# Kernel optimization log

Hardware: AMD Instinct MI355X
Metric: run time of the kernel (lower is better)

The kernel has to match this reference:

```python
import jax, jax.numpy as jnp
import numpy as np

E = 768   # embed_dim
N = 12    # num_heads
H = 128   # height
W = 128   # width
D = E // N  # head_dim = 64


def setup_inputs() -> dict:
    key = jax.random.key(0)
    ks = jax.random.split(key, 9)
    s = 0.02
    x = jax.random.normal(ks[0], (1, H * W, E), jnp.float32)
    Wq = jax.random.normal(ks[1], (E, E), jnp.float32) * s
    bq = jnp.zeros((E,), jnp.float32)
    Wk = jax.random.normal(ks[2], (E, E), jnp.float32) * s
    bk = jnp.zeros((E,), jnp.float32)
    Wv = jax.random.normal(ks[3], (E, E), jnp.float32) * s
    bv = jnp.zeros((E,), jnp.float32)
    Wo = jax.random.normal(ks[4], (E, E), jnp.float32) * s
    bo = jnp.zeros((E,), jnp.float32)
    return {"x": x, "Wq": Wq, "bq": bq, "Wk": Wk, "bk": bk,
            "Wv": Wv, "bv": bv, "Wo": Wo, "bo": bo}


def reference(x, Wq, bq, Wk, bk, Wv, bv, Wo, bo):
    # projections (torch Linear: x @ W.T + b)
    q = x @ Wq.T + bq
    k = x @ Wk.T + bk
    v = x @ Wv.T + bv

    # q, k -> (1, N, H, W, D)
    q = q.reshape(1, H, W, N, D).transpose(0, 3, 1, 2, 4)
    k = k.reshape(1, H, W, N, D).transpose(0, 3, 1, 2, 4)

    # --- width-axis attention (per row h) ---
    qr_w = q.transpose(0, 2, 1, 3, 4)  # (1, H, N, W, D)
    kr_w = k.transpose(0, 2, 1, 3, 4)  # (1, H, N, W, D)
    v = v.reshape(1, H, W, N, D).transpose(0, 1, 3, 2, 4)  # (1, H, N, W, D)
    # NOTE: original applies no 1/sqrt(D) scaling
    qk_w = jnp.einsum('bhnwd,bhnvd->bhnwv', qr_w, kr_w)  # (1, H, N, W, W)
    qk_w = jax.nn.softmax(qk_w, axis=-1)
    v = jnp.einsum('bhnwv,bhnvd->bhnwd', qk_w, v)  # (1, H, N, W, D)

    # --- height-axis attention (per column w) ---
    qr_h = q.transpose(0, 3, 1, 2, 4)  # (1, W, N, H, D)
    kr_h = k.transpose(0, 3, 1, 2, 4)  # (1, W, N, H, D)
    v = v.transpose(0, 3, 2, 1, 4)     # (1, W, N, H, D)
    qk_h = jnp.einsum('bwnhd,bwngd->bwnhg', qr_h, kr_h)  # (1, W, N, H, H)
    qk_h = jax.nn.softmax(qk_h, axis=-1)
    out = jnp.einsum('bwnhg,bwngd->bwnhd', qk_h, v)  # (1, W, N, H, D)

    # (1, W, N, H, D) -> (1, H, W, N, D) -> (1, H, W, E)
    out = out.transpose(0, 3, 1, 2, 4).reshape(1, H, W, E)
    out = out @ Wo.T + bo
    return out.reshape(1, H * W, E)
```

## Files before the change

### kernel.cpp

```cpp
#include <hip/hip_runtime.h>

typedef __attribute__((ext_vector_type(4))) float f32x4;
typedef __attribute__((ext_vector_type(8))) unsigned short u16x8;
typedef __attribute__((ext_vector_type(8))) __bf16 bf16x8;

typedef __attribute__((address_space(3))) unsigned lds_u32;
typedef const __attribute__((address_space(1))) unsigned glb_u32;

__device__ __forceinline__ unsigned short f2bf(float f) {
    union { float f; unsigned u; } v; v.f = f;
    unsigned r = v.u + 0x7fffu + ((v.u >> 16) & 1u);
    return (unsigned short)(r >> 16);
}

__device__ __forceinline__ f32x4 mfma16(u16x8 a, u16x8 b, f32x4 c) {
    return __builtin_amdgcn_mfma_f32_16x16x32_bf16(
        __builtin_bit_cast(bf16x8, a), __builtin_bit_cast(bf16x8, b), c, 0, 0, 0);
}

__device__ __forceinline__ void gload16(const unsigned short* g, unsigned short* l) {
    __builtin_amdgcn_global_load_lds((glb_u32*)g, (lds_u32*)l, 16, 0, 0);
}

#define BARM() asm volatile("s_barrier" ::: "memory")
#define WAITVM0() asm volatile("s_waitcnt vmcnt(0)" ::: "memory")

__global__ void cvt_f32_bf16(const float* __restrict__ src,
                             unsigned short* __restrict__ dst, int n) {
    int stride = gridDim.x * blockDim.x * 4;
    for (int i = (blockIdx.x * blockDim.x + threadIdx.x) * 4; i < n; i += stride) {
        float4 f = *reinterpret_cast<const float4*>(src + i);
        ushort4 o;
        o.x = f2bf(f.x); o.y = f2bf(f.y); o.z = f2bf(f.z); o.w = f2bf(f.w);
        *reinterpret_cast<ushort4*>(dst + i) = o;
    }
}

__global__ void cvt4_f32_bf16(const float* __restrict__ s0, const float* __restrict__ s1,
                              const float* __restrict__ s2, const float* __restrict__ s3,
                              unsigned short* __restrict__ dst, int per) {
    int total = per * 4;
    int stride = gridDim.x * blockDim.x * 4;
    for (int i = (blockIdx.x * blockDim.x + threadIdx.x) * 4; i < total; i += stride) {
        int w = i / per, off = i - w * per;
        const float* s = w == 0 ? s0 : w == 1 ? s1 : w == 2 ? s2 : s3;
        float4 f = *reinterpret_cast<const float4*>(s + off);
        ushort4 o;
        o.x = f2bf(f.x); o.y = f2bf(f.y); o.z = f2bf(f.z); o.w = f2bf(f.w);
        *reinterpret_cast<ushort4*>(dst + i) = o;
    }
}

template<bool OUTF32>
__device__ __forceinline__ void gemm_core(
    const unsigned short* __restrict__ A,
    const unsigned short* __restrict__ B,
    const float* __restrict__ b0, const float* __restrict__ b1, const float* __restrict__ b2,
    void* __restrict__ C0, void* __restrict__ C1, void* __restrict__ C2,
    int K, int NBY)
{
    __shared__ char lds[32768];
    const int t = threadIdx.x, lane = t & 63, wave = t >> 6;
    const int wm = wave >> 1, wn = wave & 1;

    const int nwg = gridDim.x;
    const int bid = blockIdx.x;
    const int swzb = (bid & 7) * (nwg >> 3) + (bid >> 3);
    const long m0 = (long)(swzb / NBY) * 128;
    const long n0 = (long)(swzb % NBY) * 128;

    const int NT = K >> 6;

    const int rloc = t >> 3;
    const int cel  = ((t & 7) ^ ((t >> 3) & 7)) << 3;
    const unsigned short* Ab = A + (m0 + rloc) * (long)K + cel;
    const unsigned short* Bb = B + (n0 + rloc) * (long)K + cel;

    auto STAGE = [&](int kt) {
        char* da = lds + (wave << 10);
        char* db = lds + 16384 + (wave << 10);
        const unsigned short* sa = Ab + kt * 64;
        const unsigned short* sb = Bb + kt * 64;
        #pragma unroll
        for (int j = 0; j < 4; ++j) {
            gload16(sa + (long)(j * 32) * K, (unsigned short*)(da + j * 4096));
            gload16(sb + (long)(j * 32) * K, (unsigned short*)(db + j * 4096));
        }
    };

    f32x4 acc[4][4] = {};
    u16x8 af[4][2], bfr[4][2];

    auto LD = [&]() {
        const char* bufA = lds;
        const char* bufB = lds + 16384;
        #pragma unroll
        for (int f = 0; f < 4; ++f)
            #pragma unroll
            for (int kk = 0; kk < 2; ++kk) {
                int ra = wm * 64 + f * 16 + (lane & 15);
                int rb = wn * 64 + f * 16 + (lane & 15);
                int cb = kk * 64 + (lane >> 4) * 16;
                af[f][kk]  = *(const u16x8*)(bufA + ra * 128 + (cb ^ ((ra & 7) << 4)));
                bfr[f][kk] = *(const u16x8*)(bufB + rb * 128 + (cb ^ ((rb & 7) << 4)));
            }
    };

    for (int kt = 0; kt < NT; ++kt) {
        STAGE(kt);
        WAITVM0();
        BARM();
        LD();
        #pragma unroll
        for (int kk = 0; kk < 2; ++kk)
            #pragma unroll
            for (int mi = 0; mi < 4; ++mi)
                #pragma unroll
                for (int nf = 0; nf < 4; ++nf)
                    acc[mi][nf] = mfma16(af[mi][kk], bfr[nf][kk], acc[mi][nf]);
        BARM();
    }

    #pragma unroll
    for (int mi = 0; mi < 4; ++mi)
        #pragma unroll
        for (int nf = 0; nf < 4; ++nf) {
            int coln = (int)n0 + wn * 64 + nf * 16 + (lane & 15);
            int which = coln / 768;
            int nl = coln - which * 768;
            const float* bs = which == 0 ? b0 : (which == 1 ? b1 : b2);
            void* Cp       = which == 0 ? C0 : (which == 1 ? C1 : C2);
            float bias = bs[nl];
            #pragma unroll
            for (int q = 0; q < 4; ++q) {
                long row = m0 + wm * 64 + mi * 16 + ((lane >> 4) << 2) + q;
                float val = acc[mi][nf][q] + bias;
                if (OUTF32) ((float*)Cp)[row * 768 + nl] = val;
                else ((unsigned short*)Cp)[row * 768 + nl] = f2bf(val);
            }
        }
}

__global__ __launch_bounds__(256, 4) void qkv_gemm(
    const unsigned short* __restrict__ A, const unsigned short* __restrict__ B,
    const float* b0, const float* b1, const float* b2,
    void* C0, void* C1, void* C2, int K, int NBY)
{
    gemm_core<false>(A, B, b0, b1, b2, C0, C1, C2, K, NBY);
}

__global__ __launch_bounds__(256, 4) void oproj_gemm(
    const unsigned short* __restrict__ A, const unsigned short* __restrict__ B,
    const float* b0, const float* b1, const float* b2,
    void* C0, void* C1, void* C2, int K, int NBY)
{
    gemm_core<true>(A, B, b0, b1, b2, C0, C1, C2, K, NBY);
}

__global__ __launch_bounds__(256, 3) void attn128(
    const unsigned short* __restrict__ Q,
    const unsigned short* __restrict__ K,
    const unsigned short* __restrict__ V,
    unsigned short* __restrict__ O,
    int mult, int stride)
{
    __shared__ unsigned short QK[2][128][72];
    __shared__ unsigned short Vst[64][136];
    unsigned short (*Qs)[72] = QK[0];
    unsigned short (*Ks)[72] = QK[1];
    unsigned short (*Ps)[136] = (unsigned short (*)[136])&QK[0][0][0];

    const int pos = blockIdx.x, head = blockIdx.y;
    const int t = threadIdx.x, wave = t >> 6, lane = t & 63;

    u16x8 vv[4];
    #pragma unroll
    for (int p = 0; p < 4; ++p) {
        int f = p * 2048 + t * 8;
        int r = f >> 6;
        int d = f & 63;
        long g = ((long)(pos * mult + r * stride)) * 768 + head * 64 + d;
        *(u16x8*)&Qs[r][d] = *(const u16x8*)&Q[g];
        *(u16x8*)&Ks[r][d] = *(const u16x8*)&K[g];
        vv[p] = *(const u16x8*)&V[g];
    }
    __syncthreads();

    const int rb = wave * 32;
    f32x4 s[2][8] = {};
    #pragma unroll
    for (int d0 = 0; d0 < 64; d0 += 32) {
        u16x8 a[2], b[8];
        #pragma unroll
        for (int mi = 0; mi < 2; ++mi)
            a[mi] = *(const u16x8*)&Qs[rb + mi * 16 + (lane & 15)][d0 + (lane >> 4) * 8];
        #pragma unroll
        for (int ni = 0; ni < 8; ++ni)
            b[ni] = *(const u16x8*)&Ks[ni * 16 + (lane & 15)][d0 + (lane >> 4) * 8];
        #pragma unroll
        for (int mi = 0; mi < 2; ++mi)
            #pragma unroll
            for (int ni = 0; ni < 8; ++ni)
                s[mi][ni] = mfma16(a[mi], b[ni], s[mi][ni]);
    }
    #pragma unroll
    for (int p = 0; p < 4; ++p) {
        int f = p * 2048 + t * 8;
        int r = f >> 6;
        int d = f & 63;
        #pragma unroll
        for (int j = 0; j < 8; ++j) Vst[d + j][r] = vv[p][j];
    }
    __syncthreads();

    #pragma unroll
    for (int mi = 0; mi < 2; ++mi) {
        #pragma unroll
        for (int q = 0; q < 4; ++q) {
            float m = -1e30f;
            #pragma unroll
            for (int ni = 0; ni < 8; ++ni) m = fmaxf(m, s[mi][ni][q]);
            m = fmaxf(m, __shfl_xor(m, 1));
            m = fmaxf(m, __shfl_xor(m, 2));
            m = fmaxf(m, __shfl_xor(m, 4));
            m = fmaxf(m, __shfl_xor(m, 8));
            float p[8], sum = 0.f;
            #pragma unroll
            for (int ni = 0; ni < 8; ++ni) { p[ni] = __expf(s[mi][ni][q] - m); sum += p[ni]; }
            sum += __shfl_xor(sum, 1);
            sum += __shfl_xor(sum, 2);
            sum += __shfl_xor(sum, 4);
            sum += __shfl_xor(sum, 8);
            float inv = 1.0f / sum;
            int row = rb + mi * 16 + ((lane >> 4) << 2) + q;
            #pragma unroll
            for (int ni = 0; ni < 8; ++ni)
                Ps[row][ni * 16 + (lane & 15)] = f2bf(p[ni] * inv);
        }
    }
    __syncthreads();

    f32x4 o[2][4] = {};
    #pragma unroll
    for (int v0 = 0; v0 < 128; v0 += 32) {
        u16x8 a[2], b[4];
        #pragma unroll
        for (int mi = 0; mi < 2; ++mi)
            a[mi] = *(const u16x8*)&Ps[rb + mi * 16 + (lane & 15)][v0 + (lane >> 4) * 8];
        #pragma unroll
        for (int ni = 0; ni < 4; ++ni)
            b[ni] = *(const u16x8*)&Vst[ni * 16 + (lane & 15)][v0 + (lane >> 4) * 8];
        #pragma unroll
        for (int mi = 0; mi < 2; ++mi)
            #pragma unroll
            for (int ni = 0; ni < 4; ++ni)
                o[mi][ni] = mfma16(a[mi], b[ni], o[mi][ni]);
    }

    #pragma unroll
    for (int mi = 0; mi < 2; ++mi)
        #pragma unroll
        for (int ni = 0; ni < 4; ++ni)
            #pragma unroll
            for (int q = 0; q < 4; ++q) {
                int row = rb + mi * 16 + ((lane >> 4) << 2) + q;
                int col = ni * 16 + (lane & 15);
                long g = ((long)(pos * mult + row * stride)) * 768 + head * 64 + col;
                O[g] = f2bf(o[mi][ni][q]);
            }
}

extern "C" void kernel_launch(void* const* d_in, const int* in_sizes, int n_in,
                              void* d_out, int out_size, void* d_ws, size_t ws_size,
                              hipStream_t stream) {
    const float* x  = (const float*)d_in[0];
    const float* Wq = (const float*)d_in[1];
    const float* bq = (const float*)d_in[2];
    const float* Wk = (const float*)d_in[3];
    const float* bk = (const float*)d_in[4];
    const float* Wv = (const float*)d_in[5];
    const float* bv = (const float*)d_in[6];
    const float* Wo = (const float*)d_in[7];
    const float* bo = (const float*)d_in[8];
    float* out = (float*)d_out;

    const size_t MS = (size_t)16384 * 768;
    const size_t WS = (size_t)768 * 768;
    unsigned short* xb   = (unsigned short*)d_ws;
    unsigned short* Qb   = xb + MS;
    unsigned short* Kb   = Qb + MS;
    unsigned short* Vb   = Kb + MS;
    unsigned short* Wqkv = Vb + MS;
    unsigned short* Wob  = Wqkv + 3 * WS;

    cvt_f32_bf16<<<2048, 256, 0, stream>>>(x, xb, (int)MS);
    cvt4_f32_bf16<<<2304, 256, 0, stream>>>(Wq, Wk, Wv, Wo, Wqkv, (int)WS);

    qkv_gemm<<<2304, 256, 0, stream>>>(
        xb, Wqkv, bq, bk, bv, Qb, Kb, Vb, 768, 18);

    attn128<<<dim3(128, 12), 256, 0, stream>>>(Qb, Kb, Vb, xb, 128, 1);
    attn128<<<dim3(128, 12), 256, 0, stream>>>(Qb, Kb, xb, Vb, 1, 128);

    oproj_gemm<<<768, 256, 0, stream>>>(
        Vb, Wob, bo, bo, bo, out, out, out, 768, 6);
}
```

Before: 167.7 us.

## Load Q/K MFMA fragments directly from global and merge conversion kernels

```diff
diff --git a/kernel.cpp b/kernel.cpp
--- a/kernel.cpp
+++ b/kernel.cpp
@@ -25,29 +25,28 @@
 #define BARM() asm volatile("s_barrier" ::: "memory")
 #define WAITVM0() asm volatile("s_waitcnt vmcnt(0)" ::: "memory")
 
-__global__ void cvt_f32_bf16(const float* __restrict__ src,
-                             unsigned short* __restrict__ dst, int n) {
+__global__ void cvt_all(const float* __restrict__ x,
+                        const float* __restrict__ w0, const float* __restrict__ w1,
+                        const float* __restrict__ w2, const float* __restrict__ w3,
+                        unsigned short* __restrict__ xb,
+                        unsigned short* __restrict__ wb,
+                        int nx, int perw) {
+    int total = nx + perw * 4;
     int stride = gridDim.x * blockDim.x * 4;
-    for (int i = (blockIdx.x * blockDim.x + threadIdx.x) * 4; i < n; i += stride) {
-        float4 f = *reinterpret_cast<const float4*>(src + i);
+    for (int i = (blockIdx.x * blockDim.x + threadIdx.x) * 4; i < total; i += stride) {
+        const float* s;
+        unsigned short* d;
+        if (i < nx) { s = x + i; d = xb + i; }
+        else {
+            int j = i - nx;
+            int w = j / perw, off = j - w * perw;
+            s = (w == 0 ? w0 : w == 1 ? w1 : w == 2 ? w2 : w3) + off;
+            d = wb + j;
+        }
+        float4 f = *reinterpret_cast<const float4*>(s);
         ushort4 o;
         o.x = f2bf(f.x); o.y = f2bf(f.y); o.z = f2bf(f.z); o.w = f2bf(f.w);
-        *reinterpret_cast<ushort4*>(dst + i) = o;
-    }
-}
-
-__global__ void cvt4_f32_bf16(const float* __restrict__ s0, const float* __restrict__ s1,
-                              const float* __restrict__ s2, const float* __restrict__ s3,
-                              unsigned short* __restrict__ dst, int per) {
-    int total = per * 4;
-    int stride = gridDim.x * blockDim.x * 4;
-    for (int i = (blockIdx.x * blockDim.x + threadIdx.x) * 4; i < total; i += stride) {
-        int w = i / per, off = i - w * per;
-        const float* s = w == 0 ? s0 : w == 1 ? s1 : w == 2 ? s2 : s3;
-        float4 f = *reinterpret_cast<const float4*>(s + off);
-        ushort4 o;
-        o.x = f2bf(f.x); o.y = f2bf(f.y); o.z = f2bf(f.z); o.w = f2bf(f.w);
-        *reinterpret_cast<ushort4*>(dst + i) = o;
+        *reinterpret_cast<ushort4*>(d) = o;
     }
 }
 
@@ -164,14 +163,12 @@
     unsigned short* __restrict__ O,
     int mult, int stride)
 {
-    __shared__ unsigned short QK[2][128][72];
     __shared__ unsigned short Vst[64][136];
-    unsigned short (*Qs)[72] = QK[0];
-    unsigned short (*Ks)[72] = QK[1];
-    unsigned short (*Ps)[136] = (unsigned short (*)[136])&QK[0][0][0];
+    __shared__ unsigned short Ps[128][136];
 
     const int pos = blockIdx.x, head = blockIdx.y;
     const int t = threadIdx.x, wave = t >> 6, lane = t & 63;
+    const long hbase = (long)head * 64;
 
     u16x8 vv[4];
     #pragma unroll
@@ -179,30 +176,31 @@
         int f = p * 2048 + t * 8;
         int r = f >> 6;
         int d = f & 63;
-        long g = ((long)(pos * mult + r * stride)) * 768 + head * 64 + d;
-        *(u16x8*)&Qs[r][d] = *(const u16x8*)&Q[g];
-        *(u16x8*)&Ks[r][d] = *(const u16x8*)&K[g];
-        vv[p] = *(const u16x8*)&V[g];
-    }
-    __syncthreads();
+        vv[p] = *(const u16x8*)&V[((long)(pos * mult + r * stride)) * 768 + hbase + d];
+    }
 
     const int rb = wave * 32;
+    const int c16 = lane & 15;
+    const int dof = (lane >> 4) * 8;
     f32x4 s[2][8] = {};
     #pragma unroll
     for (int d0 = 0; d0 < 64; d0 += 32) {
         u16x8 a[2], b[8];
         #pragma unroll
         for (int mi = 0; mi < 2; ++mi)
-            a[mi] = *(const u16x8*)&Qs[rb + mi * 16 + (lane & 15)][d0 + (lane >> 4) * 8];
+            a[mi] = *(const u16x8*)&Q[((long)(pos * mult + (rb + mi * 16 + c16) * stride)) * 768
+                                      + hbase + d0 + dof];
         #pragma unroll
         for (int ni = 0; ni < 8; ++ni)
-            b[ni] = *(const u16x8*)&Ks[ni * 16 + (lane & 15)][d0 + (lane >> 4) * 8];
+            b[ni] = *(const u16x8*)&K[((long)(pos * mult + (ni * 16 + c16) * stride)) * 768
+                                      + hbase + d0 + dof];
         #pragma unroll
         for (int mi = 0; mi < 2; ++mi)
             #pragma unroll
             for (int ni = 0; ni < 8; ++ni)
                 s[mi][ni] = mfma16(a[mi], b[ni], s[mi][ni]);
     }
+
     #pragma unroll
     for (int p = 0; p < 4; ++p) {
         int f = p * 2048 + t * 8;
@@ -211,7 +209,6 @@
         #pragma unroll
         for (int j = 0; j < 8; ++j) Vst[d + j][r] = vv[p][j];
     }
-    __syncthreads();
 
     #pragma unroll
     for (int mi = 0; mi < 2; ++mi) {
@@ -235,7 +232,7 @@
             int row = rb + mi * 16 + ((lane >> 4) << 2) + q;
             #pragma unroll
             for (int ni = 0; ni < 8; ++ni)
-                Ps[row][ni * 16 + (lane & 15)] = f2bf(p[ni] * inv);
+                Ps[row][ni * 16 + c16] = f2bf(p[ni] * inv);
         }
     }
     __syncthreads();
@@ -246,10 +243,10 @@
         u16x8 a[2], b[4];
         #pragma unroll
         for (int mi = 0; mi < 2; ++mi)
-            a[mi] = *(const u16x8*)&Ps[rb + mi * 16 + (lane & 15)][v0 + (lane >> 4) * 8];
+            a[mi] = *(const u16x8*)&Ps[rb + mi * 16 + c16][v0 + dof];
         #pragma unroll
         for (int ni = 0; ni < 4; ++ni)
-            b[ni] = *(const u16x8*)&Vst[ni * 16 + (lane & 15)][v0 + (lane >> 4) * 8];
+            b[ni] = *(const u16x8*)&Vst[ni * 16 + c16][v0 + dof];
         #pragma unroll
         for (int mi = 0; mi < 2; ++mi)
             #pragma unroll
@@ -264,8 +261,8 @@
             #pragma unroll
             for (int q = 0; q < 4; ++q) {
                 int row = rb + mi * 16 + ((lane >> 4) << 2) + q;
-                int col = ni * 16 + (lane & 15);
-                long g = ((long)(pos * mult + row * stride)) * 768 + head * 64 + col;
+                int col = ni * 16 + c16;
+                long g = ((long)(pos * mult + row * stride)) * 768 + hbase + col;
                 O[g] = f2bf(o[mi][ni][q]);
             }
 }
@@ -293,8 +290,8 @@
     unsigned short* Wqkv = Vb + MS;
     unsigned short* Wob  = Wqkv + 3 * WS;
 
-    cvt_f32_bf16<<<2048, 256, 0, stream>>>(x, xb, (int)MS);
-    cvt4_f32_bf16<<<2304, 256, 0, stream>>>(Wq, Wk, Wv, Wo, Wqkv, (int)WS);
+    cvt_all<<<2048, 256, 0, stream>>>(x, Wq, Wk, Wv, Wo, xb, Wqkv,
+                                      (int)MS, (int)WS);
 
     qkv_gemm<<<2304, 256, 0, stream>>>(
         xb, Wqkv, bq, bk, bv, Qb, Kb, Vb, 768, 18);
```

Result: no change. 167.6 us (-0.1%).
